# Performance work log

Measured on AMD Instinct MI355X. Metric: run time of the kernel, lower is better.

## Reference

```python
import jax, jax.numpy as jnp
import numpy as np

T, B, D_MODEL = 2048, 4, 1024
EXPAND, D_STATE, D_CONV = 2, 16, 4
D_INNER = EXPAND * D_MODEL
DT_RANK = -(-D_MODEL // 16)  # ceil(d_model/16) = 64


def setup_inputs() -> dict:
    key = jax.random.key(0)
    ks = jax.random.split(key, 10)
    g = lambda k, shape, scale: jax.random.normal(k, shape, jnp.float32) * scale
    return {
        "x": g(ks[0], (T, B, D_MODEL), 1.0),
        "W_in": g(ks[1], (D_MODEL, 2 * D_INNER), 0.02),          # in_proj (no bias)
        "conv_w": g(ks[2], (D_INNER, D_CONV), 0.2),              # depthwise conv weight
        "conv_b": g(ks[3], (D_INNER,), 0.1),                     # depthwise conv bias
        "W_x": g(ks[4], (D_INNER, DT_RANK + 2 * D_STATE), 0.02), # x_proj (no bias)
        "W_dt": g(ks[5], (DT_RANK, D_INNER), 0.05),              # dt_proj weight
        "b_dt": g(ks[6], (D_INNER,), 0.1),                       # dt_proj bias
        "A_log": jnp.log(jnp.tile(jnp.arange(1, D_STATE + 1, dtype=jnp.float32), (D_INNER, 1))),
        "D": jnp.ones((D_INNER,), jnp.float32),
        "W_out": g(ks[9], (D_INNER, D_MODEL), 0.02),             # out_proj (no bias)
    }


def reference(x, W_in, conv_w, conv_b, W_x, W_dt, b_dt, A_log, D, W_out):
    # x: (t, b, c) -> (b, t, c)
    xb = jnp.transpose(x, (1, 0, 2))
    # input projection -> (b, t, 2*d_inner), split into ssm branch u and gate res
    u, res = jnp.split(xb @ W_in, 2, axis=-1)
    # causal depthwise conv over time (torch Conv1d groups=d_inner, left pad d_conv-1)
    uc = jnp.transpose(u, (0, 2, 1))                        # (b, d_inner, t)
    uc = jax.lax.conv_general_dilated(
        uc, conv_w[:, None, :], (1,), [(D_CONV - 1, 0)],
        feature_group_count=D_INNER)
    u = jax.nn.silu(jnp.transpose(uc, (0, 2, 1)) + conv_b)  # (b, t, d_inner)
    # selective SSM parameters
    A = -jnp.exp(A_log)                                     # (d_inner, d_state)
    x_dbl = u @ W_x                                         # (b, t, dt_rank + 2n)
    delta, Bm, Cm = jnp.split(x_dbl, [DT_RANK, DT_RANK + D_STATE], axis=-1)
    delta = jax.nn.softplus(delta @ W_dt + b_dt)            # (b, t, d_inner)
    # selective scan over time; state h: (b, d_inner, d_state)
    def step(h, inp):
        d_t, B_t, C_t, u_t = inp                            # (b,d),(b,n),(b,n),(b,d)
        dA = jnp.exp(d_t[..., None] * A)                    # (b, d, n)
        h = dA * h + (d_t * u_t)[..., None] * B_t[:, None, :]
        y = jnp.einsum('bdn,bn->bd', h, C_t)
        return h, y
    h0 = jnp.zeros((B, D_INNER, D_STATE), x.dtype)
    seq = (jnp.transpose(delta, (1, 0, 2)), jnp.transpose(Bm, (1, 0, 2)),
           jnp.transpose(Cm, (1, 0, 2)), jnp.transpose(u, (1, 0, 2)))
    _, ys = jax.lax.scan(step, h0, seq)                     # (t, b, d_inner)
    y = jnp.transpose(ys, (1, 0, 2)) + u * D                # skip connection
    y = y * jax.nn.silu(res)                                # gate
    out = y @ W_out                                         # (b, t, c)
    return jnp.transpose(out, (1, 0, 2))                    # (t, b, c)
```

## Files before the change

kernel.cpp:

```cpp
#include <hip/hip_runtime.h>
#include <hip/hip_bf16.h>
#include <stdint.h>

#define T_LEN   2048
#define BATCH   4
#define DMODEL  1024
#define DINNER  2048
#define DSTATE  16
#define DTRANK  64
#define MROWS   (BATCH*T_LEN)
#define NCHUNK  16
#define CLEN    (T_LEN / NCHUNK)

typedef __bf16 bf16x8_t __attribute__((ext_vector_type(8)));
typedef float  f32x4_t  __attribute__((ext_vector_type(4)));

__device__ __forceinline__ uint16_t f2b(float f) {
    uint32_t u = __float_as_uint(f);
    u += 0x7fffu + ((u >> 16) & 1u);
    return (uint16_t)(u >> 16);
}
__device__ __forceinline__ float b2f(uint16_t h) {
    return __uint_as_float(((uint32_t)h) << 16);
}

__device__ __forceinline__ void gload16(const void* g, void* l) {
    __builtin_amdgcn_global_load_lds(
        (const __attribute__((address_space(1))) void*)g,
        (__attribute__((address_space(3))) void*)l, 16, 0, 0);
}

__global__ __launch_bounds__(256) void convert_x_kernel(
    const float* __restrict__ x, uint16_t* __restrict__ xb)
{
    int tb = blockIdx.x;
    int t = tb >> 2, b = tb & 3;
    int c = threadIdx.x * 4;
    const float4 v = *(const float4*)(x + ((size_t)tb) * DMODEL + c);
    uint16_t* dst = xb + ((size_t)(b * T_LEN + t)) * DMODEL + c;
    uint2 p;
    p.x = (uint32_t)f2b(v.x) | ((uint32_t)f2b(v.y) << 16);
    p.y = (uint32_t)f2b(v.z) | ((uint32_t)f2b(v.w) << 16);
    *(uint2*)dst = p;
}

__global__ __launch_bounds__(256) void transpose_cvt_kernel(
    const float* __restrict__ src, uint16_t* __restrict__ dst,
    int R, int C, int Cpad)
{
    __shared__ float tile[32][33];
    int r0 = blockIdx.x * 32;
    int c0 = blockIdx.y * 32;
    int tx = threadIdx.x, ty = threadIdx.y;
#pragma unroll
    for (int i = 0; i < 32; i += 8) {
        int r = r0 + ty + i, c = c0 + tx;
        tile[ty + i][tx] = (r < R && c < C) ? src[(size_t)r * C + c] : 0.f;
    }
    __syncthreads();
#pragma unroll
    for (int i = 0; i < 32; i += 8) {
        int dr = c0 + ty + i;
        int dc = r0 + tx;
        if (dr < Cpad && dc < R) dst[(size_t)dr * R + dc] = f2b(tile[tx][ty + i]);
    }
}

#define EPI_BF16  0
#define EPI_F32G  1
#define EPI_SP    2
#define EPI_REMAP 3

template <int EPI, bool SPLITK>
__global__ __launch_bounds__(256) void gemm_bt_kernel(
    const uint16_t* __restrict__ A, const uint16_t* __restrict__ Bt,
    void* __restrict__ CoutBase, const float* __restrict__ bias,
    int N, int K, int ldc, int ksplit)
{
    __shared__ uint16_t As[128 * 32];
    __shared__ uint16_t Bs[128 * 32];

    int tid = threadIdx.x;
    int bm = blockIdx.x * 128, bn = blockIdx.y * 128;
    int kbeg = SPLITK ? blockIdx.z * ksplit : 0;
    int kend = SPLITK ? kbeg + ksplit : K;
    void* Cout = SPLITK
        ? (void*)((float*)CoutBase + (size_t)blockIdx.z * MROWS * ldc)
        : CoutBase;

    const uint16_t* ap0 = A  + (size_t)(bm + (tid >> 2)) * K + kbeg + (tid & 3) * 8;
    const uint16_t* ap1 = ap0 + (size_t)64 * K;
    const uint16_t* bp0 = Bt + (size_t)(bn + (tid >> 2)) * K + kbeg + (tid & 3) * 8;
    const uint16_t* bp1 = bp0 + (size_t)64 * K;

    f32x4_t acc[4][4];
#pragma unroll
    for (int i = 0; i < 4; i++)
#pragma unroll
        for (int j = 0; j < 4; j++) acc[i][j] = (f32x4_t){0.f, 0.f, 0.f, 0.f};

    int wid = tid >> 6, lane = tid & 63;
    int wm = (wid & 1) * 64, wn = (wid >> 1) * 64;
    int lr = lane & 15, lq = lane >> 4;
    const uint16_t* Afrag = &As[(wm + lr) * 32 + lq * 8];
    const uint16_t* Bfrag = &Bs[(wn + lr) * 32 + lq * 8];

    for (int k0 = kbeg; k0 < kend; k0 += 32) {
        __syncthreads();
        gload16(ap0, &As[(size_t)tid * 8]);
        gload16(ap1, &As[(size_t)(tid + 256) * 8]);
        gload16(bp0, &Bs[(size_t)tid * 8]);
        gload16(bp1, &Bs[(size_t)(tid + 256) * 8]);
        ap0 += 32; ap1 += 32; bp0 += 32; bp1 += 32;
        __syncthreads();

        bf16x8_t av[4], bv[4];
#pragma unroll
        for (int i = 0; i < 4; i++) av[i] = *(const bf16x8_t*)(Afrag + i * 512);
#pragma unroll
        for (int j = 0; j < 4; j++) bv[j] = *(const bf16x8_t*)(Bfrag + j * 512);
#pragma unroll
        for (int i = 0; i < 4; i++)
#pragma unroll
            for (int j = 0; j < 4; j++)
                acc[i][j] = __builtin_amdgcn_mfma_f32_16x16x32_bf16(
                    av[i], bv[j], acc[i][j], 0, 0, 0);
    }

#pragma unroll
    for (int i = 0; i < 4; i++) {
#pragma unroll
        for (int j = 0; j < 4; j++) {
            int col = bn + wn + j * 16 + lr;
#pragma unroll
            for (int r = 0; r < 4; r++) {
                int row = bm + wm + i * 16 + lq * 4 + r;
                float v = acc[i][j][r];
                if (EPI == EPI_BF16) {
                    ((uint16_t*)Cout)[(size_t)row * ldc + col] = f2b(v);
                } else if (EPI == EPI_F32G) {
                    if (col < N) ((float*)Cout)[(size_t)row * ldc + col] = v;
                } else if (EPI == EPI_SP) {
                    float xv = v + bias[col];
                    float sp = (xv > 15.f) ? xv : __logf(1.f + __expf(xv));
                    ((uint16_t*)Cout)[(size_t)row * ldc + col] = f2b(sp);
                } else {
                    int bb = row >> 11, tt = row & (T_LEN - 1);
                    ((float*)Cout)[((size_t)(tt * BATCH + bb)) * ldc + col] = v;
                }
            }
        }
    }
}

#define CROWS 16

__global__ __launch_bounds__(256) void conv_silu_kernel(
    const uint16_t* __restrict__ z, const float* __restrict__ cw,
    const float* __restrict__ cb, uint16_t* __restrict__ u)
{
    int c0 = threadIdx.x * 8;
    int m0 = blockIdx.x * CROWS;

    float w[8][4], bias[8];
#pragma unroll
    for (int c = 0; c < 8; ++c)
        *(float4*)w[c] = *(const float4*)(cw + (size_t)(c0 + c) * 4);
    *(float4*)&bias[0] = *(const float4*)(cb + c0);
    *(float4*)&bias[4] = *(const float4*)(cb + c0 + 4);

    float fw[4][8];
    bool seqstart = (m0 & (T_LEN - 1)) == 0;
#pragma unroll
    for (int j = 0; j < 3; ++j) {
        int m = m0 - 3 + j;
        if (seqstart) {
#pragma unroll
            for (int c = 0; c < 8; ++c) fw[j + 1][c] = 0.f;
        } else {
            uint4 v = *(const uint4*)(z + (size_t)m * 4096 + c0);
            fw[j + 1][0] = b2f((uint16_t)(v.x & 0xffff)); fw[j + 1][1] = b2f((uint16_t)(v.x >> 16));
            fw[j + 1][2] = b2f((uint16_t)(v.y & 0xffff)); fw[j + 1][3] = b2f((uint16_t)(v.y >> 16));
            fw[j + 1][4] = b2f((uint16_t)(v.z & 0xffff)); fw[j + 1][5] = b2f((uint16_t)(v.z >> 16));
            fw[j + 1][6] = b2f((uint16_t)(v.w & 0xffff)); fw[j + 1][7] = b2f((uint16_t)(v.w >> 16));
        }
    }

#pragma unroll
    for (int t = 0; t < CROWS; ++t) {
        int m = m0 + t;
        int s = t & 3;
        uint4 v = *(const uint4*)(z + (size_t)m * 4096 + c0);
        fw[s][0] = b2f((uint16_t)(v.x & 0xffff)); fw[s][1] = b2f((uint16_t)(v.x >> 16));
        fw[s][2] = b2f((uint16_t)(v.y & 0xffff)); fw[s][3] = b2f((uint16_t)(v.y >> 16));
        fw[s][4] = b2f((uint16_t)(v.z & 0xffff)); fw[s][5] = b2f((uint16_t)(v.z >> 16));
        fw[s][6] = b2f((uint16_t)(v.w & 0xffff)); fw[s][7] = b2f((uint16_t)(v.w >> 16));
        uint16_t out[8];
#pragma unroll
        for (int c = 0; c < 8; ++c) {
            float a = bias[c];
#pragma unroll
            for (int j = 0; j < 4; ++j)
                a = fmaf(fw[(t + 1 + j) & 3][c], w[c][j], a);
            float sv = a / (1.f + __expf(-a));
            out[c] = f2b(sv);
        }
        uint4 o;
        o.x = (uint32_t)out[0] | ((uint32_t)out[1] << 16);
        o.y = (uint32_t)out[2] | ((uint32_t)out[3] << 16);
        o.z = (uint32_t)out[4] | ((uint32_t)out[5] << 16);
        o.w = (uint32_t)out[6] | ((uint32_t)out[7] << 16);
        *(uint4*)(u + (size_t)m * DINNER + c0) = o;
    }
}

__global__ __launch_bounds__(128) void reduce_xdbl_kernel(
    const float* __restrict__ xpart, float* __restrict__ xdbl,
    uint16_t* __restrict__ dr16)
{
    int m = blockIdx.x, r = threadIdx.x;
    if (r >= 96) return;
    const size_t stride = (size_t)MROWS * 96;
    size_t idx = (size_t)m * 96 + r;
    float s = xpart[idx] + xpart[stride + idx]
            + xpart[2 * stride + idx] + xpart[3 * stride + idx];
    xdbl[idx] = s;
    if (r < DTRANK) dr16[(size_t)m * DTRANK + r] = f2b(s);
}

#define LOG2E 1.44269504088896340736f

__global__ __launch_bounds__(256) void scan_part1_kernel(
    const uint16_t* __restrict__ delta16, const uint16_t* __restrict__ u16,
    const float* __restrict__ xdbl, const float* __restrict__ A_log,
    float* __restrict__ Pws, float* __restrict__ Qws)
{
    int d = blockIdx.x * 256 + threadIdx.x;
    int b = blockIdx.y;
    int c = blockIdx.z;
    float ae[DSTATE];
#pragma unroll
    for (int n = 0; n < DSTATE; ++n)
        ae[n] = -__expf(A_log[d * DSTATE + n]) * LOG2E;
    float h[DSTATE], P[DSTATE];
#pragma unroll
    for (int n = 0; n < DSTATE; ++n) { h[n] = 0.f; P[n] = 1.f; }
    size_t mbase = (size_t)b * T_LEN + (size_t)c * CLEN;

#pragma unroll 2
    for (int t = 0; t < CLEN; ++t) {
        size_t m = mbase + t;
        float delta = b2f(delta16[m * DINNER + d]);
        float du    = delta * b2f(u16[m * DINNER + d]);
        float Bv[DSTATE];
        *(float4*)&Bv[0]  = *(const float4*)(xdbl + m * 96 + 64);
        *(float4*)&Bv[4]  = *(const float4*)(xdbl + m * 96 + 68);
        *(float4*)&Bv[8]  = *(const float4*)(xdbl + m * 96 + 72);
        *(float4*)&Bv[12] = *(const float4*)(xdbl + m * 96 + 76);
#pragma unroll
        for (int n = 0; n < DSTATE; ++n) {
            float w = __builtin_amdgcn_exp2f(delta * ae[n]);
            h[n] = fmaf(w, h[n], du * Bv[n]);
            P[n] *= w;
        }
    }
    float* Pp = Pws + (((size_t)c * BATCH + b) * DINNER + d) * DSTATE;
    float* Qp = Qws + (((size_t)c * BATCH + b) * DINNER + d) * DSTATE;
#pragma unroll
    for (int n = 0; n < DSTATE; n += 4) {
        *(float4*)(Pp + n) = *(float4*)&P[n];
        *(float4*)(Qp + n) = *(float4*)&h[n];
    }
}

__global__ __launch_bounds__(256) void scan_combine_kernel(
    float* __restrict__ Pws, const float* __restrict__ Qws)
{
    size_t i = (size_t)blockIdx.x * 256 + threadIdx.x;
    const size_t stride = (size_t)BATCH * DINNER * DSTATE;
    float h = 0.f;
#pragma unroll
    for (int c = 0; c < NCHUNK; ++c) {
        float P = Pws[c * stride + i];
        float Q = Qws[c * stride + i];
        Pws[c * stride + i] = h;
        h = fmaf(P, h, Q);
    }
}

__global__ __launch_bounds__(256) void scan_part3_kernel(
    const uint16_t* __restrict__ delta16, const uint16_t* __restrict__ u16,
    const float* __restrict__ xdbl, const uint16_t* __restrict__ z16,
    const float* __restrict__ A_log, const float* __restrict__ Dvec,
    const float* __restrict__ H0ws, uint16_t* __restrict__ y16)
{
    int d = blockIdx.x * 256 + threadIdx.x;
    int b = blockIdx.y;
    int c = blockIdx.z;
    float ae[DSTATE];
#pragma unroll
    for (int n = 0; n < DSTATE; ++n)
        ae[n] = -__expf(A_log[d * DSTATE + n]) * LOG2E;
    float Dd = Dvec[d];
    float h[DSTATE];
    const float* H0p = H0ws + (((size_t)c * BATCH + b) * DINNER + d) * DSTATE;
#pragma unroll
    for (int n = 0; n < DSTATE; n += 4)
        *(float4*)&h[n] = *(const float4*)(H0p + n);
    size_t mbase = (size_t)b * T_LEN + (size_t)c * CLEN;

#pragma unroll 2
    for (int t = 0; t < CLEN; ++t) {
        size_t m = mbase + t;
        float delta = b2f(delta16[m * DINNER + d]);
        float uu    = b2f(u16[m * DINNER + d]);
        float rg    = b2f(z16[m * 4096 + DINNER + d]);
        float du    = delta * uu;
        float Bv[DSTATE], Cv[DSTATE];
        *(float4*)&Bv[0]  = *(const float4*)(xdbl + m * 96 + 64);
        *(float4*)&Bv[4]  = *(const float4*)(xdbl + m * 96 + 68);
        *(float4*)&Bv[8]  = *(const float4*)(xdbl + m * 96 + 72);
        *(float4*)&Bv[12] = *(const float4*)(xdbl + m * 96 + 76);
        *(float4*)&Cv[0]  = *(const float4*)(xdbl + m * 96 + 80);
        *(float4*)&Cv[4]  = *(const float4*)(xdbl + m * 96 + 84);
        *(float4*)&Cv[8]  = *(const float4*)(xdbl + m * 96 + 88);
        *(float4*)&Cv[12] = *(const float4*)(xdbl + m * 96 + 92);
        float y = 0.f;
#pragma unroll
        for (int n = 0; n < DSTATE; ++n) {
            float w = __builtin_amdgcn_exp2f(delta * ae[n]);
            h[n] = fmaf(w, h[n], du * Bv[n]);
            y = fmaf(h[n], Cv[n], y);
        }
        y = fmaf(uu, Dd, y);
        float sig = 1.f / (1.f + __expf(-rg));
        y16[m * DINNER + d] = f2b(y * rg * sig);
    }
}

extern "C" void kernel_launch(void* const* d_in, const int* in_sizes, int n_in,
                              void* d_out, int out_size, void* d_ws, size_t ws_size,
                              hipStream_t stream)
{
    const float* x     = (const float*)d_in[0];
    const float* W_in  = (const float*)d_in[1];
    const float* cw    = (const float*)d_in[2];
    const float* cb    = (const float*)d_in[3];
    const float* W_x   = (const float*)d_in[4];
    const float* W_dt  = (const float*)d_in[5];
    const float* b_dt  = (const float*)d_in[6];
    const float* A_log = (const float*)d_in[7];
    const float* Dv    = (const float*)d_in[8];
    const float* W_out = (const float*)d_in[9];

    char* ws = (char*)d_ws;
    size_t off = 0;
    uint16_t* xb16    = (uint16_t*)(ws + off); off += (size_t)MROWS * DMODEL * 2;
    uint16_t* WinT    = (uint16_t*)(ws + off); off += (size_t)4096 * 1024 * 2;
    uint16_t* WoutT   = (uint16_t*)(ws + off); off += (size_t)1024 * 2048 * 2;
    uint16_t* WxT     = (uint16_t*)(ws + off); off += (size_t)128 * 2048 * 2;
    uint16_t* WdtT    = (uint16_t*)(ws + off); off += (size_t)2048 * 64 * 2;
    uint16_t* z16     = (uint16_t*)(ws + off); off += (size_t)MROWS * 4096 * 2;
    uint16_t* u16     = (uint16_t*)(ws + off); off += (size_t)MROWS * DINNER * 2;
    float*    xdbl    = (float*)(ws + off);    off += (size_t)MROWS * 96 * 4;
    uint16_t* dr16    = (uint16_t*)(ws + off); off += (size_t)MROWS * 64 * 2;
    uint16_t* delta16 = (uint16_t*)(ws + off); off += (size_t)MROWS * DINNER * 2;
    uint16_t* y16     = (uint16_t*)(ws + off); off += (size_t)MROWS * DINNER * 2;

    float* xpart = (float*)xb16;
    float* Pws   = (float*)xb16;
    float* Qws   = Pws + (size_t)NCHUNK * BATCH * DINNER * DSTATE;

    dim3 tb(32, 8);
    convert_x_kernel<<<MROWS, 256, 0, stream>>>(x, xb16);
    transpose_cvt_kernel<<<dim3(32, 128), tb, 0, stream>>>(W_in,  WinT,  1024, 4096, 4096);
    transpose_cvt_kernel<<<dim3(64, 32),  tb, 0, stream>>>(W_out, WoutT, 2048, 1024, 1024);
    transpose_cvt_kernel<<<dim3(64, 4),   tb, 0, stream>>>(W_x,   WxT,   2048, 96, 128);
    transpose_cvt_kernel<<<dim3(2, 64),   tb, 0, stream>>>(W_dt,  WdtT,  64, 2048, 2048);

    gemm_bt_kernel<EPI_BF16, false><<<dim3(64, 32), 256, 0, stream>>>(
        xb16, WinT, z16, nullptr, 4096, 1024, 4096, 0);
    conv_silu_kernel<<<MROWS / CROWS, 256, 0, stream>>>(z16, cw, cb, u16);
    gemm_bt_kernel<EPI_F32G, true><<<dim3(64, 1, 4), 256, 0, stream>>>(
        u16, WxT, xpart, nullptr, 96, 2048, 96, 512);
    reduce_xdbl_kernel<<<MROWS, 128, 0, stream>>>(xpart, xdbl, dr16);
    gemm_bt_kernel<EPI_SP, false><<<dim3(64, 16), 256, 0, stream>>>(
        dr16, WdtT, delta16, b_dt, 2048, 64, 2048, 0);

    scan_part1_kernel<<<dim3(DINNER / 256, BATCH, NCHUNK), 256, 0, stream>>>(
        delta16, u16, xdbl, A_log, Pws, Qws);
    scan_combine_kernel<<<BATCH * DINNER * DSTATE / 256, 256, 0, stream>>>(
        Pws, Qws);
    scan_part3_kernel<<<dim3(DINNER / 256, BATCH, NCHUNK), 256, 0, stream>>>(
        delta16, u16, xdbl, z16, A_log, Dv, Pws, y16);

    gemm_bt_kernel<EPI_REMAP, false><<<dim3(64, 8), 256, 0, stream>>>(
        y16, WoutT, d_out, nullptr, 1024, 2048, 1024, 0);
}
```

Baseline: 482.1 us.

## Split scan state dimension across two half-wavefronts per channel

Each channel's 16 SSM states in the chunked scan kernels are now split across two lanes (the two 32-lane halves of a wavefront), each holding 8 states. This doubles the thread count and block grid for the scan phases, which raises occupancy and latency hiding on a phase that is recurrence-bound with few threads. The y output is reduced with a cross-half shuffle and only half the lanes do the gating and store. In exchange, the delta/u/z loads are duplicated across both halves and half the lanes idle during the epilogue.

```diff
diff --git a/kernel.cpp b/kernel.cpp
--- a/kernel.cpp
+++ b/kernel.cpp
@@ -235,42 +235,41 @@
     const float* __restrict__ xdbl, const float* __restrict__ A_log,
     float* __restrict__ Pws, float* __restrict__ Qws)
 {
-    int d = blockIdx.x * 256 + threadIdx.x;
+    int lane = threadIdx.x & 63;
+    int nh   = lane >> 5;
+    int nb   = nh * 8;
+    int d = blockIdx.x * 128 + (threadIdx.x >> 6) * 32 + (lane & 31);
     int b = blockIdx.y;
     int c = blockIdx.z;
-    float ae[DSTATE];
-#pragma unroll
-    for (int n = 0; n < DSTATE; ++n)
-        ae[n] = -__expf(A_log[d * DSTATE + n]) * LOG2E;
-    float h[DSTATE], P[DSTATE];
-#pragma unroll
-    for (int n = 0; n < DSTATE; ++n) { h[n] = 0.f; P[n] = 1.f; }
+    float ae[8];
+#pragma unroll
+    for (int n = 0; n < 8; ++n)
+        ae[n] = -__expf(A_log[d * DSTATE + nb + n]) * LOG2E;
+    float h[8], P[8];
+#pragma unroll
+    for (int n = 0; n < 8; ++n) { h[n] = 0.f; P[n] = 1.f; }
     size_t mbase = (size_t)b * T_LEN + (size_t)c * CLEN;
 
-#pragma unroll 2
+#pragma unroll 4
     for (int t = 0; t < CLEN; ++t) {
         size_t m = mbase + t;
         float delta = b2f(delta16[m * DINNER + d]);
         float du    = delta * b2f(u16[m * DINNER + d]);
-        float Bv[DSTATE];
-        *(float4*)&Bv[0]  = *(const float4*)(xdbl + m * 96 + 64);
-        *(float4*)&Bv[4]  = *(const float4*)(xdbl + m * 96 + 68);
-        *(float4*)&Bv[8]  = *(const float4*)(xdbl + m * 96 + 72);
-        *(float4*)&Bv[12] = *(const float4*)(xdbl + m * 96 + 76);
-#pragma unroll
-        for (int n = 0; n < DSTATE; ++n) {
+        float Bv[8];
+        *(float4*)&Bv[0] = *(const float4*)(xdbl + m * 96 + 64 + nb);
+        *(float4*)&Bv[4] = *(const float4*)(xdbl + m * 96 + 68 + nb);
+#pragma unroll
+        for (int n = 0; n < 8; ++n) {
             float w = __builtin_amdgcn_exp2f(delta * ae[n]);
             h[n] = fmaf(w, h[n], du * Bv[n]);
             P[n] *= w;
         }
     }
-    float* Pp = Pws + (((size_t)c * BATCH + b) * DINNER + d) * DSTATE;
-    float* Qp = Qws + (((size_t)c * BATCH + b) * DINNER + d) * DSTATE;
-#pragma unroll
-    for (int n = 0; n < DSTATE; n += 4) {
-        *(float4*)(Pp + n) = *(float4*)&P[n];
-        *(float4*)(Qp + n) = *(float4*)&h[n];
-    }
+    size_t base = (((size_t)c * BATCH + b) * DINNER + d) * DSTATE + nb;
+    *(float4*)(Pws + base)     = *(float4*)&P[0];
+    *(float4*)(Pws + base + 4) = *(float4*)&P[4];
+    *(float4*)(Qws + base)     = *(float4*)&h[0];
+    *(float4*)(Qws + base + 4) = *(float4*)&h[4];
 }
 
 __global__ __launch_bounds__(256) void scan_combine_kernel(
@@ -294,47 +293,48 @@
     const float* __restrict__ A_log, const float* __restrict__ Dvec,
     const float* __restrict__ H0ws, uint16_t* __restrict__ y16)
 {
-    int d = blockIdx.x * 256 + threadIdx.x;
+    int lane = threadIdx.x & 63;
+    int nh   = lane >> 5;
+    int nb   = nh * 8;
+    int d = blockIdx.x * 128 + (threadIdx.x >> 6) * 32 + (lane & 31);
     int b = blockIdx.y;
     int c = blockIdx.z;
-    float ae[DSTATE];
-#pragma unroll
-    for (int n = 0; n < DSTATE; ++n)
-        ae[n] = -__expf(A_log[d * DSTATE + n]) * LOG2E;
+    float ae[8];
+#pragma unroll
+    for (int n = 0; n < 8; ++n)
+        ae[n] = -__expf(A_log[d * DSTATE + nb + n]) * LOG2E;
     float Dd = Dvec[d];
-    float h[DSTATE];
-    const float* H0p = H0ws + (((size_t)c * BATCH + b) * DINNER + d) * DSTATE;
-#pragma unroll
-    for (int n = 0; n < DSTATE; n += 4)
-        *(float4*)&h[n] = *(const float4*)(H0p + n);
+    float h[8];
+    size_t hbase = (((size_t)c * BATCH + b) * DINNER + d) * DSTATE + nb;
+    *(float4*)&h[0] = *(const float4*)(H0ws + hbase);
+    *(float4*)&h[4] = *(const float4*)(H0ws + hbase + 4);
     size_t mbase = (size_t)b * T_LEN + (size_t)c * CLEN;
 
-#pragma unroll 2
+#pragma unroll 4
     for (int t = 0; t < CLEN; ++t) {
         size_t m = mbase + t;
         float delta = b2f(delta16[m * DINNER + d]);
         float uu    = b2f(u16[m * DINNER + d]);
         float rg    = b2f(z16[m * 4096 + DINNER + d]);
         float du    = delta * uu;
-        float Bv[DSTATE], Cv[DSTATE];
-        *(float4*)&Bv[0]  = *(const float4*)(xdbl + m * 96 + 64);
-        *(float4*)&Bv[4]  = *(const float4*)(xdbl + m * 96 + 68);
-        *(float4*)&Bv[8]  = *(const float4*)(xdbl + m * 96 + 72);
-        *(float4*)&Bv[12] = *(const float4*)(xdbl + m * 96 + 76);
-        *(float4*)&Cv[0]  = *(const float4*)(xdbl + m * 96 + 80);
-        *(float4*)&Cv[4]  = *(const float4*)(xdbl + m * 96 + 84);
-        *(float4*)&Cv[8]  = *(const float4*)(xdbl + m * 96 + 88);
-        *(float4*)&Cv[12] = *(const float4*)(xdbl + m * 96 + 92);
-        float y = 0.f;
-#pragma unroll
-        for (int n = 0; n < DSTATE; ++n) {
+        float Bv[8], Cv[8];
+        *(float4*)&Bv[0] = *(const float4*)(xdbl + m * 96 + 64 + nb);
+        *(float4*)&Bv[4] = *(const float4*)(xdbl + m * 96 + 68 + nb);
+        *(float4*)&Cv[0] = *(const float4*)(xdbl + m * 96 + 80 + nb);
+        *(float4*)&Cv[4] = *(const float4*)(xdbl + m * 96 + 84 + nb);
+        float p = 0.f;
+#pragma unroll
+        for (int n = 0; n < 8; ++n) {
             float w = __builtin_amdgcn_exp2f(delta * ae[n]);
             h[n] = fmaf(w, h[n], du * Bv[n]);
-            y = fmaf(h[n], Cv[n], y);
-        }
-        y = fmaf(uu, Dd, y);
-        float sig = 1.f / (1.f + __expf(-rg));
-        y16[m * DINNER + d] = f2b(y * rg * sig);
+            p = fmaf(h[n], Cv[n], p);
+        }
+        p += __shfl_xor(p, 32);
+        if (nh == 0) {
+            float y   = fmaf(uu, Dd, p);
+            float sig = 1.f / (1.f + __expf(-rg));
+            y16[m * DINNER + d] = f2b(y * rg * sig);
+        }
     }
 }
 
@@ -387,11 +387,11 @@
     gemm_bt_kernel<EPI_SP, false><<<dim3(64, 16), 256, 0, stream>>>(
         dr16, WdtT, delta16, b_dt, 2048, 64, 2048, 0);
 
-    scan_part1_kernel<<<dim3(DINNER / 256, BATCH, NCHUNK), 256, 0, stream>>>(
+    scan_part1_kernel<<<dim3(DINNER / 128, BATCH, NCHUNK), 256, 0, stream>>>(
         delta16, u16, xdbl, A_log, Pws, Qws);
     scan_combine_kernel<<<BATCH * DINNER * DSTATE / 256, 256, 0, stream>>>(
         Pws, Qws);
-    scan_part3_kernel<<<dim3(DINNER / 256, BATCH, NCHUNK), 256, 0, stream>>>(
+    scan_part3_kernel<<<dim3(DINNER / 128, BATCH, NCHUNK), 256, 0, stream>>>(
         delta16, u16, xdbl, z16, A_log, Dv, Pws, y16);
 
     gemm_bt_kernel<EPI_REMAP, false><<<dim3(64, 8), 256, 0, stream>>>(
```

Result: slower. 558.4 us (+15.8%).

## Use power-of-q exp trick, LDS B/C staging and register prefetch in scan

Applied to the files above, without the earlier changes.

Both scan kernels now stage the per-chunk B (and C) vectors into shared memory once per block instead of every thread reloading them from global memory. A rolling register prefetch of delta/u/gate values hides global latency. When A follows the integer pattern A[n]=(n+1)*A[0], checked at runtime, the 16 exp2 per step are replaced by one exp2 and repeated multiplies. Part1 also computes the chunk decay product P as exp2(ae*sum(delta)) instead of a running product. The power trick adds rounding error accumulated over 16 multiplies, and it depends on A_log having the arange structure (a general fallback path is kept).

```diff
diff --git a/kernel.cpp b/kernel.cpp
--- a/kernel.cpp
+++ b/kernel.cpp
@@ -11,6 +11,7 @@
 #define MROWS   (BATCH*T_LEN)
 #define NCHUNK  16
 #define CLEN    (T_LEN / NCHUNK)
+#define PF      8
 
 typedef __bf16 bf16x8_t __attribute__((ext_vector_type(8)));
 typedef float  f32x4_t  __attribute__((ext_vector_type(4)));
@@ -235,35 +236,94 @@
     const float* __restrict__ xdbl, const float* __restrict__ A_log,
     float* __restrict__ Pws, float* __restrict__ Qws)
 {
-    int d = blockIdx.x * 256 + threadIdx.x;
-    int b = blockIdx.y;
-    int c = blockIdx.z;
+    __shared__ float lds_b[CLEN][16];
+    int tid = threadIdx.x;
+    int d = blockIdx.x * 256 + tid;
+    int b = blockIdx.y, c = blockIdx.z;
+    size_t mbase = (size_t)b * T_LEN + (size_t)c * CLEN;
+
+    {
+        int r = tid >> 1, pair = tid & 1;
+        const float4* src = (const float4*)(xdbl + (mbase + r) * 96 + 64 + pair * 8);
+        float4* dst = (float4*)&lds_b[r][pair * 8];
+        dst[0] = src[0]; dst[1] = src[1];
+    }
+
     float ae[DSTATE];
 #pragma unroll
     for (int n = 0; n < DSTATE; ++n)
         ae[n] = -__expf(A_log[d * DSTATE + n]) * LOG2E;
-    float h[DSTATE], P[DSTATE];
-#pragma unroll
-    for (int n = 0; n < DSTATE; ++n) { h[n] = 0.f; P[n] = 1.f; }
-    size_t mbase = (size_t)b * T_LEN + (size_t)c * CLEN;
-
-#pragma unroll 2
-    for (int t = 0; t < CLEN; ++t) {
+    bool fastexp = true;
+#pragma unroll
+    for (int n = 1; n < DSTATE; ++n)
+        fastexp = fastexp && (fabsf(ae[n] - (n + 1) * ae[0]) <= 1e-4f * fabsf(ae[n]));
+
+    float h[DSTATE];
+#pragma unroll
+    for (int n = 0; n < DSTATE; ++n) h[n] = 0.f;
+    float sdelta = 0.f;
+
+    uint16_t dpf[PF], upf[PF];
+#pragma unroll
+    for (int t = 0; t < PF; ++t) {
         size_t m = mbase + t;
-        float delta = b2f(delta16[m * DINNER + d]);
-        float du    = delta * b2f(u16[m * DINNER + d]);
-        float Bv[DSTATE];
-        *(float4*)&Bv[0]  = *(const float4*)(xdbl + m * 96 + 64);
-        *(float4*)&Bv[4]  = *(const float4*)(xdbl + m * 96 + 68);
-        *(float4*)&Bv[8]  = *(const float4*)(xdbl + m * 96 + 72);
-        *(float4*)&Bv[12] = *(const float4*)(xdbl + m * 96 + 76);
-#pragma unroll
-        for (int n = 0; n < DSTATE; ++n) {
-            float w = __builtin_amdgcn_exp2f(delta * ae[n]);
-            h[n] = fmaf(w, h[n], du * Bv[n]);
-            P[n] *= w;
-        }
-    }
+        dpf[t] = delta16[m * DINNER + d];
+        upf[t] = u16[m * DINNER + d];
+    }
+    __syncthreads();
+
+    if (fastexp) {
+#pragma unroll 8
+        for (int t = 0; t < CLEN; ++t) {
+            int slot = t & (PF - 1);
+            float delta = b2f(dpf[slot]);
+            float du    = delta * b2f(upf[slot]);
+            int tn = t + PF; tn = tn < CLEN ? tn : CLEN - 1;
+            size_t mn = mbase + tn;
+            dpf[slot] = delta16[mn * DINNER + d];
+            upf[slot] = u16[mn * DINNER + d];
+            float Bv[DSTATE];
+            *(float4*)&Bv[0]  = *(const float4*)&lds_b[t][0];
+            *(float4*)&Bv[4]  = *(const float4*)&lds_b[t][4];
+            *(float4*)&Bv[8]  = *(const float4*)&lds_b[t][8];
+            *(float4*)&Bv[12] = *(const float4*)&lds_b[t][12];
+            float q = __builtin_amdgcn_exp2f(delta * ae[0]);
+            float w = 1.f;
+            sdelta += delta;
+#pragma unroll
+            for (int n = 0; n < DSTATE; ++n) {
+                w *= q;
+                h[n] = fmaf(w, h[n], du * Bv[n]);
+            }
+        }
+    } else {
+#pragma unroll 8
+        for (int t = 0; t < CLEN; ++t) {
+            int slot = t & (PF - 1);
+            float delta = b2f(dpf[slot]);
+            float du    = delta * b2f(upf[slot]);
+            int tn = t + PF; tn = tn < CLEN ? tn : CLEN - 1;
+            size_t mn = mbase + tn;
+            dpf[slot] = delta16[mn * DINNER + d];
+            upf[slot] = u16[mn * DINNER + d];
+            float Bv[DSTATE];
+            *(float4*)&Bv[0]  = *(const float4*)&lds_b[t][0];
+            *(float4*)&Bv[4]  = *(const float4*)&lds_b[t][4];
+            *(float4*)&Bv[8]  = *(const float4*)&lds_b[t][8];
+            *(float4*)&Bv[12] = *(const float4*)&lds_b[t][12];
+            sdelta += delta;
+#pragma unroll
+            for (int n = 0; n < DSTATE; ++n) {
+                float w = __builtin_amdgcn_exp2f(delta * ae[n]);
+                h[n] = fmaf(w, h[n], du * Bv[n]);
+            }
+        }
+    }
+
+    float P[DSTATE];
+#pragma unroll
+    for (int n = 0; n < DSTATE; ++n)
+        P[n] = __builtin_amdgcn_exp2f(ae[n] * sdelta);
     float* Pp = Pws + (((size_t)c * BATCH + b) * DINNER + d) * DSTATE;
     float* Qp = Qws + (((size_t)c * BATCH + b) * DINNER + d) * DSTATE;
 #pragma unroll
@@ -294,47 +354,112 @@
     const float* __restrict__ A_log, const float* __restrict__ Dvec,
     const float* __restrict__ H0ws, uint16_t* __restrict__ y16)
 {
-    int d = blockIdx.x * 256 + threadIdx.x;
-    int b = blockIdx.y;
-    int c = blockIdx.z;
+    __shared__ float lds_bc[CLEN][32];
+    int tid = threadIdx.x;
+    int d = blockIdx.x * 256 + tid;
+    int b = blockIdx.y, c = blockIdx.z;
+    size_t mbase = (size_t)b * T_LEN + (size_t)c * CLEN;
+
+    {
+        int r = tid >> 1, half = tid & 1;
+        const float4* src = (const float4*)(xdbl + (mbase + r) * 96 + 64 + half * 16);
+        float4* dst = (float4*)&lds_bc[r][half * 16];
+        dst[0] = src[0]; dst[1] = src[1]; dst[2] = src[2]; dst[3] = src[3];
+    }
+
     float ae[DSTATE];
 #pragma unroll
     for (int n = 0; n < DSTATE; ++n)
         ae[n] = -__expf(A_log[d * DSTATE + n]) * LOG2E;
+    bool fastexp = true;
+#pragma unroll
+    for (int n = 1; n < DSTATE; ++n)
+        fastexp = fastexp && (fabsf(ae[n] - (n + 1) * ae[0]) <= 1e-4f * fabsf(ae[n]));
     float Dd = Dvec[d];
+
     float h[DSTATE];
-    const float* H0p = H0ws + (((size_t)c * BATCH + b) * DINNER + d) * DSTATE;
+    size_t hbase = (((size_t)c * BATCH + b) * DINNER + d) * DSTATE;
 #pragma unroll
     for (int n = 0; n < DSTATE; n += 4)
-        *(float4*)&h[n] = *(const float4*)(H0p + n);
-    size_t mbase = (size_t)b * T_LEN + (size_t)c * CLEN;
-
-#pragma unroll 2
-    for (int t = 0; t < CLEN; ++t) {
+        *(float4*)&h[n] = *(const float4*)(H0ws + hbase + n);
+
+    uint16_t dpf[PF], upf[PF], rpf[PF];
+#pragma unroll
+    for (int t = 0; t < PF; ++t) {
         size_t m = mbase + t;
-        float delta = b2f(delta16[m * DINNER + d]);
-        float uu    = b2f(u16[m * DINNER + d]);
-        float rg    = b2f(z16[m * 4096 + DINNER + d]);
-        float du    = delta * uu;
-        float Bv[DSTATE], Cv[DSTATE];
-        *(float4*)&Bv[0]  = *(const float4*)(xdbl + m * 96 + 64);
-        *(float4*)&Bv[4]  = *(const float4*)(xdbl + m * 96 + 68);
-        *(float4*)&Bv[8]  = *(const float4*)(xdbl + m * 96 + 72);
-        *(float4*)&Bv[12] = *(const float4*)(xdbl + m * 96 + 76);
-        *(float4*)&Cv[0]  = *(const float4*)(xdbl + m * 96 + 80);
-        *(float4*)&Cv[4]  = *(const float4*)(xdbl + m * 96 + 84);
-        *(float4*)&Cv[8]  = *(const float4*)(xdbl + m * 96 + 88);
-        *(float4*)&Cv[12] = *(const float4*)(xdbl + m * 96 + 92);
-        float y = 0.f;
-#pragma unroll
-        for (int n = 0; n < DSTATE; ++n) {
-            float w = __builtin_amdgcn_exp2f(delta * ae[n]);
-            h[n] = fmaf(w, h[n], du * Bv[n]);
-            y = fmaf(h[n], Cv[n], y);
-        }
-        y = fmaf(uu, Dd, y);
-        float sig = 1.f / (1.f + __expf(-rg));
-        y16[m * DINNER + d] = f2b(y * rg * sig);
+        dpf[t] = delta16[m * DINNER + d];
+        upf[t] = u16[m * DINNER + d];
+        rpf[t] = z16[m * 4096 + DINNER + d];
+    }
+    __syncthreads();
+
+    if (fastexp) {
+#pragma unroll 8
+        for (int t = 0; t < CLEN; ++t) {
+            int slot = t & (PF - 1);
+            float delta = b2f(dpf[slot]);
+            float uu    = b2f(upf[slot]);
+            float rg    = b2f(rpf[slot]);
+            int tn = t + PF; tn = tn < CLEN ? tn : CLEN - 1;
+            size_t mn = mbase + tn;
+            dpf[slot] = delta16[mn * DINNER + d];
+            upf[slot] = u16[mn * DINNER + d];
+            rpf[slot] = z16[mn * 4096 + DINNER + d];
+            float du = delta * uu;
+            float Bv[DSTATE], Cv[DSTATE];
+            *(float4*)&Bv[0]  = *(const float4*)&lds_bc[t][0];
+            *(float4*)&Bv[4]  = *(const float4*)&lds_bc[t][4];
+            *(float4*)&Bv[8]  = *(const float4*)&lds_bc[t][8];
+            *(float4*)&Bv[12] = *(const float4*)&lds_bc[t][12];
+            *(float4*)&Cv[0]  = *(const float4*)&lds_bc[t][16];
+            *(float4*)&Cv[4]  = *(const float4*)&lds_bc[t][20];
+            *(float4*)&Cv[8]  = *(const float4*)&lds_bc[t][24];
+            *(float4*)&Cv[12] = *(const float4*)&lds_bc[t][28];
+            float q = __builtin_amdgcn_exp2f(delta * ae[0]);
+            float w = 1.f, y = 0.f;
+#pragma unroll
+            for (int n = 0; n < DSTATE; ++n) {
+                w *= q;
+                h[n] = fmaf(w, h[n], du * Bv[n]);
+                y = fmaf(h[n], Cv[n], y);
+            }
+            y = fmaf(uu, Dd, y);
+            float sig = 1.f / (1.f + __expf(-rg));
+            y16[(mbase + t) * DINNER + d] = f2b(y * rg * sig);
+        }
+    } else {
+#pragma unroll 8
+        for (int t = 0; t < CLEN; ++t) {
+            int slot = t & (PF - 1);
+            float delta = b2f(dpf[slot]);
+            float uu    = b2f(upf[slot]);
+            float rg    = b2f(rpf[slot]);
+            int tn = t + PF; tn = tn < CLEN ? tn : CLEN - 1;
+            size_t mn = mbase + tn;
+            dpf[slot] = delta16[mn * DINNER + d];
+            upf[slot] = u16[mn * DINNER + d];
+            rpf[slot] = z16[mn * 4096 + DINNER + d];
+            float du = delta * uu;
+            float Bv[DSTATE], Cv[DSTATE];
+            *(float4*)&Bv[0]  = *(const float4*)&lds_bc[t][0];
+            *(float4*)&Bv[4]  = *(const float4*)&lds_bc[t][4];
+            *(float4*)&Bv[8]  = *(const float4*)&lds_bc[t][8];
+            *(float4*)&Bv[12] = *(const float4*)&lds_bc[t][12];
+            *(float4*)&Cv[0]  = *(const float4*)&lds_bc[t][16];
+            *(float4*)&Cv[4]  = *(const float4*)&lds_bc[t][20];
+            *(float4*)&Cv[8]  = *(const float4*)&lds_bc[t][24];
+            *(float4*)&Cv[12] = *(const float4*)&lds_bc[t][28];
+            float y = 0.f;
+#pragma unroll
+            for (int n = 0; n < DSTATE; ++n) {
+                float w = __builtin_amdgcn_exp2f(delta * ae[n]);
+                h[n] = fmaf(w, h[n], du * Bv[n]);
+                y = fmaf(h[n], Cv[n], y);
+            }
+            y = fmaf(uu, Dd, y);
+            float sig = 1.f / (1.f + __expf(-rg));
+            y16[(mbase + t) * DINNER + d] = f2b(y * rg * sig);
+        }
     }
 }
 
```

Measured after the change: 420.2 us. 12.8% less time.
